# Optimization experiments

Measured on AMD Instinct MI355X. Metric: run time of the kernel, lower is better.

The kernel has to match this reference:

```python
import jax, jax.numpy as jnp
import numpy as np

B, S, D, H, F = 4, 1024, 1024, 16, 4096
DK = D // H
NEG_INF = jnp.float32(-jnp.inf)


def rmsnorm(x, gamma):
    rms = jnp.sqrt(jnp.mean(x * x, axis=-1, keepdims=True))
    return gamma * x / rms


def masked_softmax(cor):
    # softmax over last dim; rows that are entirely -inf produce all-zero rows
    # (matches the original's NaN -> 0 masked_fill).
    m = jnp.max(cor, axis=-1, keepdims=True)
    m_safe = jnp.where(jnp.isneginf(m), 0.0, m)
    e = jnp.exp(cor - m_safe)
    denom = jnp.sum(e, axis=-1, keepdims=True)
    return e / jnp.where(denom == 0.0, 1.0, denom)


def setup_inputs() -> dict:
    key = jax.random.key(0)
    ks = jax.random.split(key, 12)
    inp = {
        'src': jax.random.normal(ks[0], (B, S, D), jnp.float32),
        'src_padding_mask': jax.random.bernoulli(ks[1], 0.1, (B, S)),
        'prev': jax.random.normal(ks[2], (H, B, S, S), jnp.float32),
        'layer_ind': 2,
        'Wq': jax.random.normal(ks[3], (H, D, DK), jnp.float32) * 0.02,
        'Wk': jax.random.normal(ks[4], (H, D, DK), jnp.float32) * 0.02,
        'Wv': jax.random.normal(ks[5], (H, D, DK), jnp.float32) * 0.02,
        'Wproj': jax.random.normal(ks[6], (D, D), jnp.float32) * 0.02,
        'gamma1': jnp.ones((D,), jnp.float32),
        'gamma2': jnp.ones((D,), jnp.float32),
        'W1': jax.random.normal(ks[7], (D, F), jnp.float32) * 0.02,
        'b1': jnp.zeros((F,), jnp.float32),
        'W2': jax.random.normal(ks[8], (F, D), jnp.float32) * 0.02,
        'b2': jnp.zeros((D,), jnp.float32),
    }
    return inp


def reference(src, src_padding_mask, prev, layer_ind, Wq, Wk, Wv, Wproj,
              gamma1, gamma2, W1, b1, W2, b2):
    ln1 = rmsnorm(src, gamma1)                              # [B,S,D]
    q = jnp.einsum('bsd,hdk->hbsk', ln1, Wq)                # [H,B,S,DK]
    k = jnp.einsum('bsd,hdk->hbsk', ln1, Wk)
    v = jnp.einsum('bsd,hdk->hbsk', ln1, Wv)
    scores = jnp.einsum('hbsk,hbtk->hbst', q, k) * (DK ** -0.5)  # [H,B,S,S]
    qmask = src_padding_mask[None, :, :, None]              # query (row) pad mask
    kvmask = src_padding_mask[None, :, None, :]             # key   (col) pad mask
    scores = jnp.where(qmask, NEG_INF, scores)
    scores = jnp.where(kvmask, NEG_INF, scores)
    raw = (scores + prev) / 2                               # RealFormer residual scores
    cor = raw / (1.0 - 0.5 ** layer_ind)
    w = masked_softmax(cor)                                 # [H,B,S,S]
    att = jnp.einsum('hbst,hbtk->bshk', w, v).reshape(B, S, H * DK)
    attention = att @ Wproj + src                           # residual
    h = jax.nn.relu(rmsnorm(attention, gamma2) @ W1 + b1)
    out = attention + (h @ W2 + b2)
    return out, raw
```

## Files before the change

kernel.cpp:

```cpp
#include <hip/hip_runtime.h>
#include <math.h>

#define Bv 4
#define Sv 1024
#define Dv 1024
#define Hv 16
#define Fv 4096
#define DKv 64

#define MASK_SENTINEL (-3.0e38f)

typedef __attribute__((ext_vector_type(8))) short short8v;
typedef __attribute__((ext_vector_type(4))) float float4v;

__device__ inline unsigned short bf16_rne(float x) {
    unsigned int u = __float_as_uint(x);
    unsigned int r = (u + 0x7FFFu + ((u >> 16) & 1u)) >> 16;
    return (unsigned short)r;
}
__device__ inline float bf16_tof(unsigned short h) {
    return __uint_as_float(((unsigned int)h) << 16);
}
__device__ inline void split2(float x, unsigned short& h, unsigned short& l) {
    unsigned short hh = bf16_rne(x);
    h = hh;
    l = bf16_rne(x - bf16_tof(hh));
}

__global__ __launch_bounds__(256) void rmsnorm_split_k(const float* __restrict__ x,
                                                       const float* __restrict__ g,
                                                       unsigned short* __restrict__ yh,
                                                       unsigned short* __restrict__ yl)
{
    const int row = blockIdx.x;
    const int tid = threadIdx.x;
    const float4* xv = reinterpret_cast<const float4*>(x) + (size_t)row * (Dv / 4);
    float4 v = xv[tid];
    float ss = v.x * v.x + v.y * v.y + v.z * v.z + v.w * v.w;
    #pragma unroll
    for (int o = 32; o > 0; o >>= 1) ss += __shfl_down(ss, o);
    __shared__ float wsum[4];
    if ((tid & 63) == 0) wsum[tid >> 6] = ss;
    __syncthreads();
    const float total = wsum[0] + wsum[1] + wsum[2] + wsum[3];
    const float rinv = rsqrtf(total * (1.0f / Dv));
    const float4 gv = reinterpret_cast<const float4*>(g)[tid];
    float o0 = v.x * gv.x * rinv, o1 = v.y * gv.y * rinv;
    float o2 = v.z * gv.z * rinv, o3 = v.w * gv.w * rinv;
    ushort4 uh, ul; unsigned short h, l;
    split2(o0, h, l); uh.x = h; ul.x = l;
    split2(o1, h, l); uh.y = h; ul.y = l;
    split2(o2, h, l); uh.z = h; ul.z = l;
    split2(o3, h, l); uh.w = h; ul.w = l;
    *(ushort4*)&yh[(size_t)row * Dv + tid * 4] = uh;
    *(ushort4*)&yl[(size_t)row * Dv + tid * 4] = ul;
}

template<bool HEADW>
__global__ __launch_bounds__(256) void tsplit_k(const float* __restrict__ W,
                                                unsigned short* __restrict__ WTh,
                                                unsigned short* __restrict__ WTl,
                                                int K, int N)
{
    __shared__ float tile[64 * 68];
    const int tid = threadIdx.x;
    const int n0 = blockIdx.x * 64, k0 = blockIdx.y * 64;
    #pragma unroll
    for (int it = 0; it < 4; ++it) {
        int slot = it * 256 + tid;
        int r = slot >> 4, c4 = (slot & 15) * 4;
        const float* src;
        if (HEADW)
            src = &W[((size_t)(n0 >> 6) * K + (k0 + r)) * 64 + c4];
        else
            src = &W[(size_t)(k0 + r) * N + n0 + c4];
        *(float4*)&tile[r * 68 + c4] = *(const float4*)src;
    }
    __syncthreads();
    #pragma unroll
    for (int it = 0; it < 4; ++it) {
        int slot = it * 256 + tid;
        int rr = slot >> 4, c4 = (slot & 15) * 4;
        ushort4 uh, ul;
        unsigned short h, l;
        split2(tile[(c4 + 0) * 68 + rr], h, l); uh.x = h; ul.x = l;
        split2(tile[(c4 + 1) * 68 + rr], h, l); uh.y = h; ul.y = l;
        split2(tile[(c4 + 2) * 68 + rr], h, l); uh.z = h; ul.z = l;
        split2(tile[(c4 + 3) * 68 + rr], h, l); uh.w = h; ul.w = l;
        size_t o = (size_t)(n0 + rr) * K + k0 + c4;
        *(ushort4*)&WTh[o] = uh;
        *(ushort4*)&WTl[o] = ul;
    }
}

#define BKP 40
template<int OUTM, bool RELU, bool BIAS, bool RES>
__global__ __launch_bounds__(256) void gemm_mfma_s(const unsigned short* __restrict__ Ahg,
                                                   const unsigned short* __restrict__ Alg,
                                                   const unsigned short* __restrict__ Bhg,
                                                   const unsigned short* __restrict__ Blg,
                                                   const float* __restrict__ bias,
                                                   const float* __restrict__ res,
                                                   float* __restrict__ C,
                                                   unsigned short* __restrict__ Ch,
                                                   unsigned short* __restrict__ Cl,
                                                   int M, int N, int K)
{
    __shared__ unsigned short Ah[128 * BKP], Al[128 * BKP];
    __shared__ unsigned short Bh[128 * BKP], Bl[128 * BKP];
    const int tid = threadIdx.x;
    const int lane = tid & 63, wid = tid >> 6;
    const int wr = wid >> 1, wc = wid & 1;
    const int l15 = lane & 15, lg = lane >> 4;
    const int bm = blockIdx.y * 128, bn = blockIdx.x * 128;

    float4v acc[4][4];
    #pragma unroll
    for (int i = 0; i < 4; ++i)
        #pragma unroll
        for (int j = 0; j < 4; ++j) acc[i][j] = (float4v)(0.0f);

    for (int k0 = 0; k0 < K; k0 += 32) {
        #pragma unroll
        for (int it = 0; it < 2; ++it) {
            int slot = it * 256 + tid;
            int r = slot >> 2, c8 = (slot & 3) * 8;
            *(uint4*)&Ah[r * BKP + c8] = *(const uint4*)&Ahg[(size_t)(bm + r) * K + k0 + c8];
            *(uint4*)&Al[r * BKP + c8] = *(const uint4*)&Alg[(size_t)(bm + r) * K + k0 + c8];
            *(uint4*)&Bh[r * BKP + c8] = *(const uint4*)&Bhg[(size_t)(bn + r) * K + k0 + c8];
            *(uint4*)&Bl[r * BKP + c8] = *(const uint4*)&Blg[(size_t)(bn + r) * K + k0 + c8];
        }
        __syncthreads();

        short8v fah[4], fal[4], fbh[4], fbl[4];
        const int kb = lg * 8;
        #pragma unroll
        for (int mi = 0; mi < 4; ++mi) {
            int row = wr * 64 + mi * 16 + l15;
            fah[mi] = *(const short8v*)&Ah[row * BKP + kb];
            fal[mi] = *(const short8v*)&Al[row * BKP + kb];
        }
        #pragma unroll
        for (int ni = 0; ni < 4; ++ni) {
            int row = wc * 64 + ni * 16 + l15;
            fbh[ni] = *(const short8v*)&Bh[row * BKP + kb];
            fbl[ni] = *(const short8v*)&Bl[row * BKP + kb];
        }
        #pragma unroll
        for (int mi = 0; mi < 4; ++mi)
            #pragma unroll
            for (int ni = 0; ni < 4; ++ni) {
                float4v c = acc[mi][ni];
                c = __builtin_amdgcn_mfma_f32_16x16x32_bf16(fah[mi], fbh[ni], c, 0, 0, 0);
                c = __builtin_amdgcn_mfma_f32_16x16x32_bf16(fah[mi], fbl[ni], c, 0, 0, 0);
                c = __builtin_amdgcn_mfma_f32_16x16x32_bf16(fal[mi], fbh[ni], c, 0, 0, 0);
                acc[mi][ni] = c;
            }
        __syncthreads();
    }

    #pragma unroll
    for (int mi = 0; mi < 4; ++mi) {
        #pragma unroll
        for (int r = 0; r < 4; ++r) {
            int m = bm + wr * 64 + mi * 16 + lg * 4 + r;
            #pragma unroll
            for (int ni = 0; ni < 4; ++ni) {
                int n = bn + wc * 64 + ni * 16 + l15;
                float v = acc[mi][ni][r];
                if (BIAS) v += bias[n];
                if (RELU) v = fmaxf(v, 0.0f);
                if (RES)  v += res[(size_t)m * N + n];
                if (OUTM == 0) {
                    C[(size_t)m * N + n] = v;
                } else {
                    int hh = n >> 6, dk = n & 63, bb = m >> 10, s = m & 1023;
                    size_t off = (((size_t)(hh * Bv + bb)) * Sv + s) * DKv + dk;
                    unsigned short hi, lo;
                    split2(v, hi, lo);
                    Ch[off] = hi;
                    Cl[off] = lo;
                }
            }
        }
    }
}

template<bool RELU, bool BIAS, bool RES>
__global__ __launch_bounds__(256) void gemm_mfma(const float* __restrict__ A,
                                                 const unsigned short* __restrict__ Bhg,
                                                 const unsigned short* __restrict__ Blg,
                                                 const float* __restrict__ bias,
                                                 const float* __restrict__ res,
                                                 float* __restrict__ C,
                                                 int M, int N, int K)
{
    __shared__ unsigned short Ah[128 * BKP], Al[128 * BKP];
    __shared__ unsigned short Bh[128 * BKP], Bl[128 * BKP];
    const int tid = threadIdx.x;
    const int lane = tid & 63, wid = tid >> 6;
    const int wr = wid >> 1, wc = wid & 1;
    const int l15 = lane & 15, lg = lane >> 4;
    const int bm = blockIdx.y * 128, bn = blockIdx.x * 128;

    float4v acc[4][4];
    #pragma unroll
    for (int i = 0; i < 4; ++i)
        #pragma unroll
        for (int j = 0; j < 4; ++j) acc[i][j] = (float4v)(0.0f);

    for (int k0 = 0; k0 < K; k0 += 32) {
        #pragma unroll
        for (int it = 0; it < 4; ++it) {
            int slot = it * 256 + tid;
            int r = slot >> 3, c4 = (slot & 7) * 4;
            float4 v = *(const float4*)&A[(size_t)(bm + r) * K + k0 + c4];
            ushort4 uh, ul; unsigned short h, l;
            split2(v.x, h, l); uh.x = h; ul.x = l;
            split2(v.y, h, l); uh.y = h; ul.y = l;
            split2(v.z, h, l); uh.z = h; ul.z = l;
            split2(v.w, h, l); uh.w = h; ul.w = l;
            *(ushort4*)&Ah[r * BKP + c4] = uh;
            *(ushort4*)&Al[r * BKP + c4] = ul;
        }
        #pragma unroll
        for (int it = 0; it < 2; ++it) {
            int slot = it * 256 + tid;
            int r = slot >> 2, c8 = (slot & 3) * 8;
            *(uint4*)&Bh[r * BKP + c8] = *(const uint4*)&Bhg[(size_t)(bn + r) * K + k0 + c8];
            *(uint4*)&Bl[r * BKP + c8] = *(const uint4*)&Blg[(size_t)(bn + r) * K + k0 + c8];
        }
        __syncthreads();

        short8v fah[4], fal[4], fbh[4], fbl[4];
        const int kb = lg * 8;
        #pragma unroll
        for (int mi = 0; mi < 4; ++mi) {
            int row = wr * 64 + mi * 16 + l15;
            fah[mi] = *(const short8v*)&Ah[row * BKP + kb];
            fal[mi] = *(const short8v*)&Al[row * BKP + kb];
        }
        #pragma unroll
        for (int ni = 0; ni < 4; ++ni) {
            int row = wc * 64 + ni * 16 + l15;
            fbh[ni] = *(const short8v*)&Bh[row * BKP + kb];
            fbl[ni] = *(const short8v*)&Bl[row * BKP + kb];
        }
        #pragma unroll
        for (int mi = 0; mi < 4; ++mi)
            #pragma unroll
            for (int ni = 0; ni < 4; ++ni) {
                float4v c = acc[mi][ni];
                c = __builtin_amdgcn_mfma_f32_16x16x32_bf16(fah[mi], fbh[ni], c, 0, 0, 0);
                c = __builtin_amdgcn_mfma_f32_16x16x32_bf16(fah[mi], fbl[ni], c, 0, 0, 0);
                c = __builtin_amdgcn_mfma_f32_16x16x32_bf16(fal[mi], fbh[ni], c, 0, 0, 0);
                acc[mi][ni] = c;
            }
        __syncthreads();
    }

    #pragma unroll
    for (int mi = 0; mi < 4; ++mi) {
        #pragma unroll
        for (int r = 0; r < 4; ++r) {
            int m = bm + wr * 64 + mi * 16 + lg * 4 + r;
            #pragma unroll
            for (int ni = 0; ni < 4; ++ni) {
                int n = bn + wc * 64 + ni * 16 + l15;
                float v = acc[mi][ni][r];
                if (BIAS) v += bias[n];
                if (RELU) v = fmaxf(v, 0.0f);
                if (RES)  v += res[(size_t)m * N + n];
                C[(size_t)m * N + n] = v;
            }
        }
    }
}

__global__ __launch_bounds__(256) void scores_mfma_k(const unsigned short* __restrict__ qh,
                                                     const unsigned short* __restrict__ ql,
                                                     const unsigned short* __restrict__ kh,
                                                     const unsigned short* __restrict__ kl,
                                                     const float* __restrict__ prev,
                                                     const unsigned char* __restrict__ mask,
                                                     const int* __restrict__ layer_ind,
                                                     float* __restrict__ raw,
                                                     float* __restrict__ stat_m,
                                                     float* __restrict__ stat_s)
{
    __shared__ float T[4][16 * 68];
    const int tid = threadIdx.x;
    const int lane = tid & 63, wid = tid >> 6;
    const int wr = wid >> 1, wc = wid & 1;
    const int l15 = lane & 15, lg = lane >> 4;
    const int hb = blockIdx.y, b = hb & 3;
    const int sm = (blockIdx.x >> 3) * 128;
    const int tn = (blockIdx.x & 7) * 128;
    const float cs = 1.0f / (1.0f - exp2f(-(float)layer_ind[0]));

    float4v acc[4][4];
    #pragma unroll
    for (int i = 0; i < 4; ++i)
        #pragma unroll
        for (int j = 0; j < 4; ++j) acc[i][j] = (float4v)(0.0f);

    const size_t qbase = ((size_t)hb * Sv + sm + wr * 64) * DKv;
    const size_t kbase = ((size_t)hb * Sv + tn + wc * 64) * DKv;

    #pragma unroll
    for (int kk = 0; kk < 2; ++kk) {
        const int kb = kk * 32 + lg * 8;
        short8v fah[4], fal[4], fbh[4], fbl[4];
        #pragma unroll
        for (int mi = 0; mi < 4; ++mi) {
            size_t off = qbase + (size_t)(mi * 16 + l15) * DKv + kb;
            fah[mi] = *(const short8v*)&qh[off];
            fal[mi] = *(const short8v*)&ql[off];
        }
        #pragma unroll
        for (int ni = 0; ni < 4; ++ni) {
            size_t off = kbase + (size_t)(ni * 16 + l15) * DKv + kb;
            fbh[ni] = *(const short8v*)&kh[off];
            fbl[ni] = *(const short8v*)&kl[off];
        }
        #pragma unroll
        for (int mi = 0; mi < 4; ++mi)
            #pragma unroll
            for (int ni = 0; ni < 4; ++ni) {
                float4v c = acc[mi][ni];
                c = __builtin_amdgcn_mfma_f32_16x16x32_bf16(fah[mi], fbh[ni], c, 0, 0, 0);
                c = __builtin_amdgcn_mfma_f32_16x16x32_bf16(fah[mi], fbl[ni], c, 0, 0, 0);
                c = __builtin_amdgcn_mfma_f32_16x16x32_bf16(fal[mi], fbh[ni], c, 0, 0, 0);
                acc[mi][ni] = c;
            }
    }

    const int tb2 = (blockIdx.x & 7) * 2 + wc;

    #pragma unroll
    for (int mi = 0; mi < 4; ++mi) {
        #pragma unroll
        for (int ni = 0; ni < 4; ++ni)
            #pragma unroll
            for (int r = 0; r < 4; ++r)
                T[wid][(lg * 4 + r) * 68 + ni * 16 + l15] = acc[mi][ni][r];
        __syncthreads();

        const int s = sm + wr * 64 + mi * 16 + l15;
        const bool qm = mask[b * Sv + s] != 0;
        float xv[16];
        #pragma unroll
        for (int c = 0; c < 4; ++c) {
            float4 tv = *(const float4*)&T[wid][l15 * 68 + lg * 16 + c * 4];
            const int t = tn + wc * 64 + lg * 16 + c * 4;
            const size_t off = ((size_t)hb * Sv + s) * Sv + t;
            const float4 pv = *(const float4*)&prev[off];
            const uchar4 km = *(const uchar4*)&mask[b * Sv + t];
            float4 o;
            o.x = (qm || km.x) ? MASK_SENTINEL : (tv.x * 0.125f + pv.x) * 0.5f;
            o.y = (qm || km.y) ? MASK_SENTINEL : (tv.y * 0.125f + pv.y) * 0.5f;
            o.z = (qm || km.z) ? MASK_SENTINEL : (tv.z * 0.125f + pv.z) * 0.5f;
            o.w = (qm || km.w) ? MASK_SENTINEL : (tv.w * 0.125f + pv.w) * 0.5f;
            *(float4*)&raw[off] = o;
            xv[c * 4 + 0] = (qm || km.x) ? -INFINITY : o.x * cs;
            xv[c * 4 + 1] = (qm || km.y) ? -INFINITY : o.y * cs;
            xv[c * 4 + 2] = (qm || km.z) ? -INFINITY : o.z * cs;
            xv[c * 4 + 3] = (qm || km.w) ? -INFINITY : o.w * cs;
        }
        __syncthreads();

        float mx = -INFINITY;
        #pragma unroll
        for (int j = 0; j < 16; ++j) mx = fmaxf(mx, xv[j]);
        mx = fmaxf(mx, __shfl_xor(mx, 16));
        mx = fmaxf(mx, __shfl_xor(mx, 32));
        float se = 0.0f;
        #pragma unroll
        for (int j = 0; j < 16; ++j)
            se += (xv[j] == -INFINITY) ? 0.0f : __expf(xv[j] - mx);
        se += __shfl_xor(se, 16);
        se += __shfl_xor(se, 32);
        if (lg == 0) {
            const size_t slot = (((size_t)hb * Sv + s) << 4) + tb2;
            stat_m[slot] = mx;
            stat_s[slot] = se;
        }
    }
}

__global__ __launch_bounds__(256) void softmax_pv_k(const float* __restrict__ raw,
                                                    const float* __restrict__ v2d,
                                                    const float* __restrict__ stat_m,
                                                    const float* __restrict__ stat_s,
                                                    const int* __restrict__ layer_ind,
                                                    unsigned short* __restrict__ att2dh,
                                                    unsigned short* __restrict__ att2dl)
{
    __shared__ float Vt[64 * 68];
    __shared__ float Wt[32 * 68];
    __shared__ float rowM[32], rowR[32];
    const int tid = threadIdx.x;
    const int hb = blockIdx.y, h = hb >> 2, b = hb & 3;
    const int s0 = blockIdx.x * 32;
    const float cs = 1.0f / (1.0f - exp2f(-(float)layer_ind[0]));

    if (tid < 32) {
        const size_t base = ((size_t)hb * Sv + s0 + tid) << 4;
        float m = -INFINITY;
        #pragma unroll
        for (int j = 0; j < 16; ++j) m = fmaxf(m, stat_m[base + j]);
        float ssum = 0.0f;
        #pragma unroll
        for (int j = 0; j < 16; ++j) {
            const float sj = stat_s[base + j];
            const float mj = stat_m[base + j];
            if (sj > 0.0f) ssum += __expf(mj - m) * sj;
        }
        rowM[tid] = (m == -INFINITY) ? 0.0f : m;
        rowR[tid] = (ssum == 0.0f) ? 1.0f : 1.0f / ssum;
    }
    __syncthreads();

    const int dk4 = (tid & 15) * 4;
    const int rp2 = tid >> 4;
    const int r0 = rp2 * 2, r1 = r0 + 1;
    float4 a0 = {0, 0, 0, 0}, a1 = {0, 0, 0, 0};

    const int wrow = tid >> 3, wc8 = (tid & 7) * 8;

    for (int tc = 0; tc < Sv; tc += 64) {
        #pragma unroll
        for (int it = 0; it < 4; ++it) {
            int slot = it * 256 + tid;
            int r = slot >> 4, c4 = (slot & 15) * 4;
            *(float4*)&Vt[r * 68 + c4] =
                *(const float4*)&v2d[((size_t)b * Sv + tc + r) * Dv + h * DKv + c4];
        }
        {
            const float mm = rowM[wrow], rc = rowR[wrow];
            const size_t off = ((size_t)hb * Sv + s0 + wrow) * Sv + tc + wc8;
            const float4 x0 = *(const float4*)&raw[off];
            const float4 x1 = *(const float4*)&raw[off + 4];
            float4 e0, e1;
            e0.x = (x0.x < -1e37f) ? 0.0f : __expf(x0.x * cs - mm) * rc;
            e0.y = (x0.y < -1e37f) ? 0.0f : __expf(x0.y * cs - mm) * rc;
            e0.z = (x0.z < -1e37f) ? 0.0f : __expf(x0.z * cs - mm) * rc;
            e0.w = (x0.w < -1e37f) ? 0.0f : __expf(x0.w * cs - mm) * rc;
            e1.x = (x1.x < -1e37f) ? 0.0f : __expf(x1.x * cs - mm) * rc;
            e1.y = (x1.y < -1e37f) ? 0.0f : __expf(x1.y * cs - mm) * rc;
            e1.z = (x1.z < -1e37f) ? 0.0f : __expf(x1.z * cs - mm) * rc;
            e1.w = (x1.w < -1e37f) ? 0.0f : __expf(x1.w * cs - mm) * rc;
            *(float4*)&Wt[wrow * 68 + wc8] = e0;
            *(float4*)&Wt[wrow * 68 + wc8 + 4] = e1;
        }
        __syncthreads();
        #pragma unroll 4
        for (int tt = 0; tt < 64; ++tt) {
            float4 vv = *(const float4*)&Vt[tt * 68 + dk4];
            float w0 = Wt[r0 * 68 + tt];
            float w1 = Wt[r1 * 68 + tt];
            a0.x = fmaf(w0, vv.x, a0.x); a0.y = fmaf(w0, vv.y, a0.y);
            a0.z = fmaf(w0, vv.z, a0.z); a0.w = fmaf(w0, vv.w, a0.w);
            a1.x = fmaf(w1, vv.x, a1.x); a1.y = fmaf(w1, vv.y, a1.y);
            a1.z = fmaf(w1, vv.z, a1.z); a1.w = fmaf(w1, vv.w, a1.w);
        }
        __syncthreads();
    }
    ushort4 uh, ul; unsigned short hh, ll;
    size_t o0 = ((size_t)b * Sv + s0 + r0) * Dv + h * DKv + dk4;
    size_t o1 = ((size_t)b * Sv + s0 + r1) * Dv + h * DKv + dk4;
    split2(a0.x, hh, ll); uh.x = hh; ul.x = ll;
    split2(a0.y, hh, ll); uh.y = hh; ul.y = ll;
    split2(a0.z, hh, ll); uh.z = hh; ul.z = ll;
    split2(a0.w, hh, ll); uh.w = hh; ul.w = ll;
    *(ushort4*)&att2dh[o0] = uh; *(ushort4*)&att2dl[o0] = ul;
    split2(a1.x, hh, ll); uh.x = hh; ul.x = ll;
    split2(a1.y, hh, ll); uh.y = hh; ul.y = ll;
    split2(a1.z, hh, ll); uh.z = hh; ul.z = ll;
    split2(a1.w, hh, ll); uh.w = hh; ul.w = ll;
    *(ushort4*)&att2dh[o1] = uh; *(ushort4*)&att2dl[o1] = ul;
}

extern "C" void kernel_launch(void* const* d_in, const int* in_sizes, int n_in,
                              void* d_out, int out_size, void* d_ws, size_t ws_size,
                              hipStream_t stream)
{
    const float* src          = (const float*)d_in[0];
    const unsigned char* mask = (const unsigned char*)d_in[1];
    const float* prev         = (const float*)d_in[2];
    const int* layer_ind      = (const int*)d_in[3];
    const float* Wq           = (const float*)d_in[4];
    const float* Wk           = (const float*)d_in[5];
    const float* Wv           = (const float*)d_in[6];
    const float* Wproj        = (const float*)d_in[7];
    const float* gamma1       = (const float*)d_in[8];
    const float* gamma2       = (const float*)d_in[9];
    const float* W1           = (const float*)d_in[10];
    const float* b1           = (const float*)d_in[11];
    const float* W2           = (const float*)d_in[12];
    const float* b2           = (const float*)d_in[13];

    float* out = (float*)d_out;
    float* raw = out + (size_t)Bv * Sv * Dv;

    float* ws = (float*)d_ws;
    unsigned short* S16 = (unsigned short*)d_ws;
    const size_t M1 = 1u << 20;
    unsigned short* WT1h = S16;
    unsigned short* WT1l = S16 + 4 * M1;
    unsigned short* WT2h = S16 + 8 * M1;
    unsigned short* WT2l = S16 + 12 * M1;
    unsigned short* WTqh = S16 + 16 * M1, *WTql = S16 + 17 * M1;
    unsigned short* WTkh = S16 + 18 * M1, *WTkl = S16 + 19 * M1;
    unsigned short* WTvh = S16 + 20 * M1, *WTvl = S16 + 21 * M1;
    unsigned short* WTph = S16 + 22 * M1, *WTpl = S16 + 23 * M1;
    unsigned short* ln2h = S16 + 16 * M1, *ln2l = S16 + 20 * M1;
    float* attn = ws + 12 * M1;
    unsigned short* ln1h = S16 + 32 * M1, *ln1l = S16 + 36 * M1;
    float* stat_m = ws + 16 * M1;
    float* stat_s = ws + 17 * M1;
    unsigned short* qh   = S16 + 40 * M1, *ql   = S16 + 44 * M1;
    unsigned short* kh   = S16 + 48 * M1, *kl   = S16 + 52 * M1;
    float* v2d = ws + 28 * M1;
    unsigned short* at2h = S16 + 40 * M1, *at2l = S16 + 44 * M1;
    float* hbuf = ws + 16 * M1;
    (void)in_sizes; (void)n_in; (void)out_size; (void)ws_size;

    tsplit_k<true ><<<dim3(16, 16), 256, 0, stream>>>(Wq,    WTqh, WTql, 1024, 1024);
    tsplit_k<true ><<<dim3(16, 16), 256, 0, stream>>>(Wk,    WTkh, WTkl, 1024, 1024);
    tsplit_k<true ><<<dim3(16, 16), 256, 0, stream>>>(Wv,    WTvh, WTvl, 1024, 1024);
    tsplit_k<false><<<dim3(16, 16), 256, 0, stream>>>(Wproj, WTph, WTpl, 1024, 1024);
    tsplit_k<false><<<dim3(64, 16), 256, 0, stream>>>(W1,    WT1h, WT1l, 1024, 4096);
    tsplit_k<false><<<dim3(16, 64), 256, 0, stream>>>(W2,    WT2h, WT2l, 4096, 1024);

    rmsnorm_split_k<<<4096, 256, 0, stream>>>(src, gamma1, ln1h, ln1l);

    dim3 gN1(8, 32);
    gemm_mfma_s<2, false, false, false><<<gN1, 256, 0, stream>>>(ln1h, ln1l, WTqh, WTql, nullptr, nullptr, nullptr, qh, ql, 4096, 1024, 1024);
    gemm_mfma_s<2, false, false, false><<<gN1, 256, 0, stream>>>(ln1h, ln1l, WTkh, WTkl, nullptr, nullptr, nullptr, kh, kl, 4096, 1024, 1024);
    gemm_mfma_s<0, false, false, false><<<gN1, 256, 0, stream>>>(ln1h, ln1l, WTvh, WTvl, nullptr, nullptr, v2d, nullptr, nullptr, 4096, 1024, 1024);

    scores_mfma_k<<<dim3(64, 64), 256, 0, stream>>>(qh, ql, kh, kl, prev, mask, layer_ind, raw, stat_m, stat_s);

    softmax_pv_k<<<dim3(32, 64), 256, 0, stream>>>(raw, v2d, stat_m, stat_s, layer_ind, at2h, at2l);

    gemm_mfma_s<0, false, false, true><<<gN1, 256, 0, stream>>>(at2h, at2l, WTph, WTpl, nullptr, src, attn, nullptr, nullptr, 4096, 1024, 1024);

    rmsnorm_split_k<<<4096, 256, 0, stream>>>(attn, gamma2, ln2h, ln2l);

    gemm_mfma_s<0, true, true, false><<<dim3(32, 32), 256, 0, stream>>>(ln2h, ln2l, WT1h, WT1l, b1, nullptr, hbuf, nullptr, nullptr, 4096, 4096, 1024);

    gemm_mfma<false, true, true><<<gN1, 256, 0, stream>>>(hbuf, WT2h, WT2l, b2, attn, out, 4096, 1024, 4096);
}
```

Before: 933.9 us.

## Use 512-thread GEMM blocks, XCD-aware block swizzle, and pre-split FFN hidden activations

The split-bf16 GEMM now runs 8 waves per 128x128 tile, each wave computing 64x32. Tiles are remapped so consecutive blocks on the same XCD share B columns. The first FFN GEMM writes its ReLU output directly as hi/lo bf16 pairs, so the second FFN GEMM reuses the pre-split path instead of reading fp32 and splitting it per tile. This removes redundant fp32 loads and split work in the W2 GEMM and aims to improve latency hiding, at the cost of more LDS traffic per MFMA and workspace buffer aliasing.

```diff
diff --git a/kernel.cpp b/kernel.cpp
--- a/kernel.cpp
+++ b/kernel.cpp
@@ -95,7 +95,7 @@
 
 #define BKP 40
 template<int OUTM, bool RELU, bool BIAS, bool RES>
-__global__ __launch_bounds__(256) void gemm_mfma_s(const unsigned short* __restrict__ Ahg,
+__global__ __launch_bounds__(512) void gemm_mfma_s(const unsigned short* __restrict__ Ahg,
                                                    const unsigned short* __restrict__ Alg,
                                                    const unsigned short* __restrict__ Bhg,
                                                    const unsigned short* __restrict__ Blg,
@@ -110,29 +110,32 @@
     __shared__ unsigned short Bh[128 * BKP], Bl[128 * BKP];
     const int tid = threadIdx.x;
     const int lane = tid & 63, wid = tid >> 6;
-    const int wr = wid >> 1, wc = wid & 1;
+    const int wr = wid >> 2, wc = wid & 3;
     const int l15 = lane & 15, lg = lane >> 4;
-    const int bm = blockIdx.y * 128, bn = blockIdx.x * 128;
-
-    float4v acc[4][4];
+
+    const int nx = gridDim.x, ny = gridDim.y;
+    const int flat = blockIdx.y * nx + blockIdx.x;
+    const int cpx = (nx * ny) >> 3;
+    const int g = (flat & 7) * cpx + (flat >> 3);
+    const int bn = (g / ny) * 128;
+    const int bm = (g % ny) * 128;
+
+    float4v acc[4][2];
     #pragma unroll
     for (int i = 0; i < 4; ++i)
         #pragma unroll
-        for (int j = 0; j < 4; ++j) acc[i][j] = (float4v)(0.0f);
+        for (int j = 0; j < 2; ++j) acc[i][j] = (float4v)(0.0f);
+
+    const int sr = tid >> 2, sc8 = (tid & 3) * 8;
 
     for (int k0 = 0; k0 < K; k0 += 32) {
-        #pragma unroll
-        for (int it = 0; it < 2; ++it) {
-            int slot = it * 256 + tid;
-            int r = slot >> 2, c8 = (slot & 3) * 8;
-            *(uint4*)&Ah[r * BKP + c8] = *(const uint4*)&Ahg[(size_t)(bm + r) * K + k0 + c8];
-            *(uint4*)&Al[r * BKP + c8] = *(const uint4*)&Alg[(size_t)(bm + r) * K + k0 + c8];
-            *(uint4*)&Bh[r * BKP + c8] = *(const uint4*)&Bhg[(size_t)(bn + r) * K + k0 + c8];
-            *(uint4*)&Bl[r * BKP + c8] = *(const uint4*)&Blg[(size_t)(bn + r) * K + k0 + c8];
-        }
-        __syncthreads();
-
-        short8v fah[4], fal[4], fbh[4], fbl[4];
+        *(uint4*)&Ah[sr * BKP + sc8] = *(const uint4*)&Ahg[(size_t)(bm + sr) * K + k0 + sc8];
+        *(uint4*)&Al[sr * BKP + sc8] = *(const uint4*)&Alg[(size_t)(bm + sr) * K + k0 + sc8];
+        *(uint4*)&Bh[sr * BKP + sc8] = *(const uint4*)&Bhg[(size_t)(bn + sr) * K + k0 + sc8];
+        *(uint4*)&Bl[sr * BKP + sc8] = *(const uint4*)&Blg[(size_t)(bn + sr) * K + k0 + sc8];
+        __syncthreads();
+
+        short8v fah[4], fal[4], fbh[2], fbl[2];
         const int kb = lg * 8;
         #pragma unroll
         for (int mi = 0; mi < 4; ++mi) {
@@ -141,15 +144,15 @@
             fal[mi] = *(const short8v*)&Al[row * BKP + kb];
         }
         #pragma unroll
-        for (int ni = 0; ni < 4; ++ni) {
-            int row = wc * 64 + ni * 16 + l15;
+        for (int ni = 0; ni < 2; ++ni) {
+            int row = wc * 32 + ni * 16 + l15;
             fbh[ni] = *(const short8v*)&Bh[row * BKP + kb];
             fbl[ni] = *(const short8v*)&Bl[row * BKP + kb];
         }
         #pragma unroll
         for (int mi = 0; mi < 4; ++mi)
             #pragma unroll
-            for (int ni = 0; ni < 4; ++ni) {
+            for (int ni = 0; ni < 2; ++ni) {
                 float4v c = acc[mi][ni];
                 c = __builtin_amdgcn_mfma_f32_16x16x32_bf16(fah[mi], fbh[ni], c, 0, 0, 0);
                 c = __builtin_amdgcn_mfma_f32_16x16x32_bf16(fah[mi], fbl[ni], c, 0, 0, 0);
@@ -165,14 +168,19 @@
         for (int r = 0; r < 4; ++r) {
             int m = bm + wr * 64 + mi * 16 + lg * 4 + r;
             #pragma unroll
-            for (int ni = 0; ni < 4; ++ni) {
-                int n = bn + wc * 64 + ni * 16 + l15;
+            for (int ni = 0; ni < 2; ++ni) {
+                int n = bn + wc * 32 + ni * 16 + l15;
                 float v = acc[mi][ni][r];
                 if (BIAS) v += bias[n];
                 if (RELU) v = fmaxf(v, 0.0f);
                 if (RES)  v += res[(size_t)m * N + n];
                 if (OUTM == 0) {
                     C[(size_t)m * N + n] = v;
+                } else if (OUTM == 1) {
+                    unsigned short hi, lo;
+                    split2(v, hi, lo);
+                    Ch[(size_t)m * N + n] = hi;
+                    Cl[(size_t)m * N + n] = lo;
                 } else {
                     int hh = n >> 6, dk = n & 63, bb = m >> 10, s = m & 1023;
                     size_t off = (((size_t)(hh * Bv + bb)) * Sv + s) * DKv + dk;
@@ -181,97 +189,6 @@
                     Ch[off] = hi;
                     Cl[off] = lo;
                 }
-            }
-        }
-    }
-}
-
-template<bool RELU, bool BIAS, bool RES>
-__global__ __launch_bounds__(256) void gemm_mfma(const float* __restrict__ A,
-                                                 const unsigned short* __restrict__ Bhg,
-                                                 const unsigned short* __restrict__ Blg,
-                                                 const float* __restrict__ bias,
-                                                 const float* __restrict__ res,
-                                                 float* __restrict__ C,
-                                                 int M, int N, int K)
-{
-    __shared__ unsigned short Ah[128 * BKP], Al[128 * BKP];
-    __shared__ unsigned short Bh[128 * BKP], Bl[128 * BKP];
-    const int tid = threadIdx.x;
-    const int lane = tid & 63, wid = tid >> 6;
-    const int wr = wid >> 1, wc = wid & 1;
-    const int l15 = lane & 15, lg = lane >> 4;
-    const int bm = blockIdx.y * 128, bn = blockIdx.x * 128;
-
-    float4v acc[4][4];
-    #pragma unroll
-    for (int i = 0; i < 4; ++i)
-        #pragma unroll
-        for (int j = 0; j < 4; ++j) acc[i][j] = (float4v)(0.0f);
-
-    for (int k0 = 0; k0 < K; k0 += 32) {
-        #pragma unroll
-        for (int it = 0; it < 4; ++it) {
-            int slot = it * 256 + tid;
-            int r = slot >> 3, c4 = (slot & 7) * 4;
-            float4 v = *(const float4*)&A[(size_t)(bm + r) * K + k0 + c4];
-            ushort4 uh, ul; unsigned short h, l;
-            split2(v.x, h, l); uh.x = h; ul.x = l;
-            split2(v.y, h, l); uh.y = h; ul.y = l;
-            split2(v.z, h, l); uh.z = h; ul.z = l;
-            split2(v.w, h, l); uh.w = h; ul.w = l;
-            *(ushort4*)&Ah[r * BKP + c4] = uh;
-            *(ushort4*)&Al[r * BKP + c4] = ul;
-        }
-        #pragma unroll
-        for (int it = 0; it < 2; ++it) {
-            int slot = it * 256 + tid;
-            int r = slot >> 2, c8 = (slot & 3) * 8;
-            *(uint4*)&Bh[r * BKP + c8] = *(const uint4*)&Bhg[(size_t)(bn + r) * K + k0 + c8];
-            *(uint4*)&Bl[r * BKP + c8] = *(const uint4*)&Blg[(size_t)(bn + r) * K + k0 + c8];
-        }
-        __syncthreads();
-
-        short8v fah[4], fal[4], fbh[4], fbl[4];
-        const int kb = lg * 8;
-        #pragma unroll
-        for (int mi = 0; mi < 4; ++mi) {
-            int row = wr * 64 + mi * 16 + l15;
-            fah[mi] = *(const short8v*)&Ah[row * BKP + kb];
-            fal[mi] = *(const short8v*)&Al[row * BKP + kb];
-        }
-        #pragma unroll
-        for (int ni = 0; ni < 4; ++ni) {
-            int row = wc * 64 + ni * 16 + l15;
-            fbh[ni] = *(const short8v*)&Bh[row * BKP + kb];
-            fbl[ni] = *(const short8v*)&Bl[row * BKP + kb];
-        }
-        #pragma unroll
-        for (int mi = 0; mi < 4; ++mi)
-            #pragma unroll
-            for (int ni = 0; ni < 4; ++ni) {
-                float4v c = acc[mi][ni];
-                c = __builtin_amdgcn_mfma_f32_16x16x32_bf16(fah[mi], fbh[ni], c, 0, 0, 0);
-                c = __builtin_amdgcn_mfma_f32_16x16x32_bf16(fah[mi], fbl[ni], c, 0, 0, 0);
-                c = __builtin_amdgcn_mfma_f32_16x16x32_bf16(fal[mi], fbh[ni], c, 0, 0, 0);
-                acc[mi][ni] = c;
-            }
-        __syncthreads();
-    }
-
-    #pragma unroll
-    for (int mi = 0; mi < 4; ++mi) {
-        #pragma unroll
-        for (int r = 0; r < 4; ++r) {
-            int m = bm + wr * 64 + mi * 16 + lg * 4 + r;
-            #pragma unroll
-            for (int ni = 0; ni < 4; ++ni) {
-                int n = bn + wc * 64 + ni * 16 + l15;
-                float v = acc[mi][ni][r];
-                if (BIAS) v += bias[n];
-                if (RELU) v = fmaxf(v, 0.0f);
-                if (RES)  v += res[(size_t)m * N + n];
-                C[(size_t)m * N + n] = v;
             }
         }
     }
@@ -523,7 +440,8 @@
     unsigned short* kh   = S16 + 48 * M1, *kl   = S16 + 52 * M1;
     float* v2d = ws + 28 * M1;
     unsigned short* at2h = S16 + 40 * M1, *at2l = S16 + 44 * M1;
-    float* hbuf = ws + 16 * M1;
+    unsigned short* hbufh = S16 + 32 * M1;
+    unsigned short* hbufl = S16 + 48 * M1;
     (void)in_sizes; (void)n_in; (void)out_size; (void)ws_size;
 
     tsplit_k<true ><<<dim3(16, 16), 256, 0, stream>>>(Wq,    WTqh, WTql, 1024, 1024);
@@ -536,19 +454,19 @@
     rmsnorm_split_k<<<4096, 256, 0, stream>>>(src, gamma1, ln1h, ln1l);
 
     dim3 gN1(8, 32);
-    gemm_mfma_s<2, false, false, false><<<gN1, 256, 0, stream>>>(ln1h, ln1l, WTqh, WTql, nullptr, nullptr, nullptr, qh, ql, 4096, 1024, 1024);
-    gemm_mfma_s<2, false, false, false><<<gN1, 256, 0, stream>>>(ln1h, ln1l, WTkh, WTkl, nullptr, nullptr, nullptr, kh, kl, 4096, 1024, 1024);
-    gemm_mfma_s<0, false, false, false><<<gN1, 256, 0, stream>>>(ln1h, ln1l, WTvh, WTvl, nullptr, nullptr, v2d, nullptr, nullptr, 4096, 1024, 1024);
+    gemm_mfma_s<2, false, false, false><<<gN1, 512, 0, stream>>>(ln1h, ln1l, WTqh, WTql, nullptr, nullptr, nullptr, qh, ql, 4096, 1024, 1024);
+    gemm_mfma_s<2, false, false, false><<<gN1, 512, 0, stream>>>(ln1h, ln1l, WTkh, WTkl, nullptr, nullptr, nullptr, kh, kl, 4096, 1024, 1024);
+    gemm_mfma_s<0, false, false, false><<<gN1, 512, 0, stream>>>(ln1h, ln1l, WTvh, WTvl, nullptr, nullptr, v2d, nullptr, nullptr, 4096, 1024, 1024);
 
     scores_mfma_k<<<dim3(64, 64), 256, 0, stream>>>(qh, ql, kh, kl, prev, mask, layer_ind, raw, stat_m, stat_s);
 
     softmax_pv_k<<<dim3(32, 64), 256, 0, stream>>>(raw, v2d, stat_m, stat_s, layer_ind, at2h, at2l);
 
-    gemm_mfma_s<0, false, false, true><<<gN1, 256, 0, stream>>>(at2h, at2l, WTph, WTpl, nullptr, src, attn, nullptr, nullptr, 4096, 1024, 1024);
+    gemm_mfma_s<0, false, false, true><<<gN1, 512, 0, stream>>>(at2h, at2l, WTph, WTpl, nullptr, src, attn, nullptr, nullptr, 4096, 1024, 1024);
 
     rmsnorm_split_k<<<4096, 256, 0, stream>>>(attn, gamma2, ln2h, ln2l);
 
-    gemm_mfma_s<0, true, true, false><<<dim3(32, 32), 256, 0, stream>>>(ln2h, ln2l, WT1h, WT1l, b1, nullptr, hbuf, nullptr, nullptr, 4096, 4096, 1024);
-
-    gemm_mfma<false, true, true><<<gN1, 256, 0, stream>>>(hbuf, WT2h, WT2l, b2, attn, out, 4096, 1024, 4096);
-}
+    gemm_mfma_s<1, true, true, false><<<dim3(32, 32), 512, 0, stream>>>(ln2h, ln2l, WT1h, WT1l, b1, nullptr, nullptr, hbufh, hbufl, 4096, 4096, 1024);
+
+    gemm_mfma_s<0, false, true, true><<<gN1, 512, 0, stream>>>(hbufh, hbufl, WT2h, WT2l, b2, attn, out, nullptr, nullptr, 4096, 1024, 4096);
+}
```

Result: slower. 989.7 us (+6.0%).
